# Optimization experiments

Measured on AMD Instinct MI355X. Metric: run time of the kernel, lower is better.

## Reference

```python
import jax, jax.numpy as jnp
import numpy as np

B, L, D, H = 2, 2048, 1024, 16
DH = D // H  # 64
SIGMA = float(np.sqrt(DH))  # sigma=None, learnable_sigma=False -> sqrt(d_head)


def setup_inputs() -> dict:
    key = jax.random.key(0)
    ks = jax.random.split(key, 5)
    x = jax.random.normal(ks[0], (B, L, D), dtype=jnp.float32)
    # causal visibility mask (1 = visible, 0 = masked), [B,1,L,L]
    mask = jnp.broadcast_to(jnp.tril(jnp.ones((L, L), jnp.int32))[None, None], (B, 1, L, L))
    scale = 0.02
    W_q = jax.random.normal(ks[1], (D, D), dtype=jnp.float32) * scale
    W_k = jax.random.normal(ks[2], (D, D), dtype=jnp.float32) * scale
    W_v = jax.random.normal(ks[3], (D, D), dtype=jnp.float32) * scale
    W_o = jax.random.normal(ks[4], (D, D), dtype=jnp.float32) * scale
    return {"x": x, "mask": mask, "W_q": W_q, "W_k": W_k, "W_v": W_v, "W_o": W_o}


def _split_heads(t):
    # [B,L,D] -> [B,H,L,DH]
    b, l, _ = t.shape
    return t.reshape(b, l, H, DH).transpose(0, 2, 1, 3)


def reference(x, mask, W_q, W_k, W_v, W_o):
    # nn.Linear(bias=False): y = x @ W.T
    Qh = _split_heads(x @ W_q.T)  # [B,H,L,DH]
    Kh = _split_heads(x @ W_k.T)
    Vh = _split_heads(x @ W_v.T)
    # RBF scores: -||q-k||^2 / (2 sigma^2)
    q_norm2 = jnp.sum(Qh * Qh, axis=-1, keepdims=True)          # [B,H,L,1]
    k_norm2 = jnp.sum(Kh * Kh, axis=-1)[..., None, :]            # [B,H,1,L]
    dot_qk = jnp.einsum('bhqd,bhkd->bhqk', Qh, Kh)               # [B,H,L,L]
    dist2 = q_norm2 + k_norm2 - 2.0 * dot_qk
    scores = -dist2 / (2.0 * SIGMA * SIGMA)
    scores = jnp.where(mask == 0, -jnp.inf, scores)
    attn = jax.nn.softmax(scores, axis=-1)
    Oh = jnp.einsum('bhqk,bhkd->bhqd', attn, Vh)                 # [B,H,L,DH]
    O = Oh.transpose(0, 2, 1, 3).reshape(B, L, D)
    return O @ W_o.T
```

## Files before the change

### kernel.cpp

```cpp
#include <hip/hip_runtime.h>

#define L_SEQ  2048
#define D_MODEL 1024
#define NH 16
#define DHEAD 64
#define BATCH 2

typedef __attribute__((ext_vector_type(8))) short bf16x8;
typedef __attribute__((ext_vector_type(4))) float f32x4;

__device__ inline ushort f2bf(float f) {
  unsigned int u = __builtin_bit_cast(unsigned int, f);
  return (ushort)((u + 0x7FFFu + ((u >> 16) & 1u)) >> 16);
}
__device__ inline float bf2f(ushort u) {
  return __builtin_bit_cast(float, (unsigned int)u << 16);
}

__device__ __forceinline__ void gload_lds16(const void* g, void* l) {
  __builtin_amdgcn_global_load_lds(
      (const __attribute__((address_space(1))) void*)g,
      (__attribute__((address_space(3))) void*)l, 16, 0, 0);
}

#define PROJ8 524288
#define WSZ8  131072
__global__ __launch_bounds__(256) void cvt_all(const float* __restrict__ x,
                                               const float* __restrict__ w0,
                                               const float* __restrict__ w1,
                                               const float* __restrict__ w2,
                                               const float* __restrict__ w3,
                                               ushort* __restrict__ xb,
                                               ushort* __restrict__ ob0,
                                               ushort* __restrict__ ob1,
                                               ushort* __restrict__ ob2,
                                               ushort* __restrict__ ob3) {
  const int gid = blockIdx.x * 256 + threadIdx.x;
  const float* in; ushort* out; int off;
  if (gid < PROJ8) { in = x; out = xb; off = gid; }
  else {
    const int j = gid - PROJ8;
    const int seg = j / WSZ8;
    off = j - seg * WSZ8;
    switch (seg) {
      case 0: in = w0; out = ob0; break;
      case 1: in = w1; out = ob1; break;
      case 2: in = w2; out = ob2; break;
      default: in = w3; out = ob3; break;
    }
  }
  const float4* p = (const float4*)in + (size_t)off * 2;
  const float4 a = p[0], b = p[1];
  ushort4 lo, hi;
  lo.x = f2bf(a.x); lo.y = f2bf(a.y); lo.z = f2bf(a.z); lo.w = f2bf(a.w);
  hi.x = f2bf(b.x); hi.y = f2bf(b.y); hi.z = f2bf(b.z); hi.w = f2bf(b.w);
  ((ushort4*)out)[(size_t)off * 2] = lo;
  ((ushort4*)out)[(size_t)off * 2 + 1] = hi;
}

__global__ __launch_bounds__(512, 2) void gemm8p(const ushort* __restrict__ A,
    const ushort* __restrict__ W0, const ushort* __restrict__ W1,
    const ushort* __restrict__ W2, ushort* __restrict__ Qb,
    ushort* __restrict__ Kb, ushort* __restrict__ Vtb) {
  __shared__ ushort As[2][2][128][64];
  __shared__ ushort Bs[2][2][128][64];
  const int tid = threadIdx.x;
  const int wid = tid >> 6, l = tid & 63, lr = l & 15, lg = l >> 4;
  const int wr = wid >> 2, wc = wid & 3;

  const int bid = blockIdx.x;
  const int swz = (bid & 7) * 24 + (bid >> 3);
  const int mt = swz / 12, nt_ = swz % 12;
  const int m0g = mt * 256;
  const ushort* W = (nt_ < 4) ? W0 : (nt_ < 8) ? W1 : W2;
  ushort* outQK = (nt_ < 4) ? Qb : Kb;
  const int mode2 = (nt_ >= 8);
  const int ncol0 = (nt_ & 3) * 256;

  const int srow = tid >> 3;
  const int schunk = (tid & 7) ^ (srow & 7);
  const ushort* Ag = A + (size_t)(m0g + srow) * D_MODEL + schunk * 8;
  const ushort* Wg = W + (size_t)(ncol0 + srow) * D_MODEL + schunk * 8;
  ushort* AsL = &As[0][0][0][0] + tid * 8;
  ushort* BsL = &Bs[0][0][0][0] + tid * 8;

#define STG_A(sl, h, T2)                                                        \
  {                                                                             \
    gload_lds16(Ag + (size_t)((h) * 128) * D_MODEL + (T2) * 64,                 \
                AsL + (sl) * 16384 + (h) * 8192);                               \
    gload_lds16(Ag + (size_t)((h) * 128 + 64) * D_MODEL + (T2) * 64,            \
                AsL + (sl) * 16384 + (h) * 8192 + 4096);                        \
  }
#define STG_B(sl, h, T2)                                                        \
  {                                                                             \
    gload_lds16(Wg + (size_t)((h) * 128) * D_MODEL + (T2) * 64,                 \
                BsL + (sl) * 16384 + (h) * 8192);                               \
    gload_lds16(Wg + (size_t)((h) * 128 + 64) * D_MODEL + (T2) * 64,            \
                BsL + (sl) * 16384 + (h) * 8192 + 4096);                        \
  }

  STG_A(0, 0, 0); STG_A(0, 1, 0); STG_B(0, 0, 0); STG_B(0, 1, 0);

  f32x4 acc[8][4] = {};
  bf16x8 bfr[4][2];
  const int NT = D_MODEL / 64;

#define PHASE(q)                                                                \
  {                                                                             \
    bf16x8 af[2][2];                                                            \
    _Pragma("unroll") for (int m2 = 0; m2 < 2; ++m2)                            \
      _Pragma("unroll") for (int kk = 0; kk < 2; ++kk)                          \
        af[m2][kk] = *(const bf16x8*)&As[s][wr][((q) * 2 + m2) * 16 + lr]       \
                                           [((kk * 4 + lg) ^ (lr & 7)) * 8];    \
    if (T + 1 < NT) {                                                           \
      if ((q) == 1)      { STG_A(s ^ 1, 1, T + 1); }                            \
      else if ((q) == 2) { STG_B(s ^ 1, 0, T + 1); }                            \
      else               { STG_B(s ^ 1, 1, T + 1); }                            \
    }                                                                           \
    __builtin_amdgcn_s_barrier();                                               \
    __builtin_amdgcn_s_setprio(1);                                              \
    _Pragma("unroll") for (int m2 = 0; m2 < 2; ++m2)                            \
      _Pragma("unroll") for (int kk = 0; kk < 2; ++kk)                          \
        _Pragma("unroll") for (int n = 0; n < 4; ++n)                           \
          acc[(q) * 2 + m2][n] = __builtin_amdgcn_mfma_f32_16x16x32_bf16(       \
              af[m2][kk], bfr[n][kk], acc[(q) * 2 + m2][n], 0, 0, 0);           \
    __builtin_amdgcn_s_setprio(0);                                              \
    __builtin_amdgcn_s_barrier();                                               \
  }

  for (int T = 0; T < NT; ++T) {
    const int s = T & 1;
    {
      if (T + 1 < NT) {
        STG_A(s ^ 1, 0, T + 1);
        asm volatile("s_waitcnt vmcnt(2)" ::: "memory");
      } else {
        asm volatile("s_waitcnt vmcnt(0)" ::: "memory");
      }
      __builtin_amdgcn_s_barrier();
#pragma unroll
      for (int n = 0; n < 4; ++n)
#pragma unroll
        for (int kk = 0; kk < 2; ++kk)
          bfr[n][kk] = *(const bf16x8*)&Bs[s][wc >> 1][(wc & 1) * 64 + n * 16 + lr]
                                          [((kk * 4 + lg) ^ (lr & 7)) * 8];
      bf16x8 af[2][2];
#pragma unroll
      for (int m2 = 0; m2 < 2; ++m2)
#pragma unroll
        for (int kk = 0; kk < 2; ++kk)
          af[m2][kk] = *(const bf16x8*)&As[s][wr][m2 * 16 + lr]
                                          [((kk * 4 + lg) ^ (lr & 7)) * 8];
      __builtin_amdgcn_s_setprio(1);
#pragma unroll
      for (int m2 = 0; m2 < 2; ++m2)
#pragma unroll
        for (int kk = 0; kk < 2; ++kk)
#pragma unroll
          for (int n = 0; n < 4; ++n)
            acc[m2][n] = __builtin_amdgcn_mfma_f32_16x16x32_bf16(
                af[m2][kk], bfr[n][kk], acc[m2][n], 0, 0, 0);
      __builtin_amdgcn_s_setprio(0);
      __builtin_amdgcn_s_barrier();
    }
    PHASE(1)
    PHASE(2)
    PHASE(3)
  }
#undef PHASE
#undef STG_A
#undef STG_B

  const int h = (nt_ & 3) * 4 + wc;
  if (!mode2) {
#pragma unroll
    for (int m = 0; m < 8; ++m)
#pragma unroll
      for (int r = 0; r < 4; ++r) {
        const int grow = m0g + wr * 128 + m * 16 + lg * 4 + r;
        const int b = grow >> 11, ll = grow & (L_SEQ - 1);
        ushort* dst = outQK + ((size_t)(b * NH + h) * L_SEQ + ll) * DHEAD;
#pragma unroll
        for (int n = 0; n < 4; ++n) dst[n * 16 + lr] = f2bf(acc[m][n][r]);
      }
  } else {
#pragma unroll
    for (int m = 0; m < 8; ++m) {
      const int grow0 = m0g + wr * 128 + m * 16 + lg * 4;
      const int b = grow0 >> 11, ll = grow0 & (L_SEQ - 1);
#pragma unroll
      for (int n = 0; n < 4; ++n) {
        ushort4 v;
        v.x = f2bf(acc[m][n][0]); v.y = f2bf(acc[m][n][1]);
        v.z = f2bf(acc[m][n][2]); v.w = f2bf(acc[m][n][3]);
        *(ushort4*)(Vtb + ((size_t)(b * NH + h) * DHEAD + n * 16 + lr) * L_SEQ + ll) = v;
      }
    }
  }
}

__global__ __launch_bounds__(256) void gemm128(const ushort* __restrict__ A,
    const ushort* __restrict__ W0, float* __restrict__ of) {
  __shared__ ushort As[2][128][32];
  __shared__ ushort Bs[2][128][32];
  const int tid = threadIdx.x;
  const int w = tid >> 6, l = tid & 63, lr = l & 15, lg = l >> 4;
  const int wr = w >> 1, wc = w & 1;

  const int cpx = gridDim.x >> 3;
  const int swz = (blockIdx.x & 7) * cpx + (blockIdx.x >> 3);
  const int ntile = swz % 8;
  const int m0 = (swz / 8) * 128;
  const int n0 = ntile * 128;

  const int srow = tid >> 2;
  const int skc_sw = (tid & 3) ^ (srow & 3);
  const ushort* Ag = A + (size_t)(m0 + srow) * D_MODEL + skc_sw * 8;
  const ushort* Wg = W0 + (size_t)(n0 + srow) * D_MODEL + skc_sw * 8;

#define STAGE(buf, k0)                                                      \
  {                                                                         \
    gload_lds16(Ag + (k0), &As[buf][0][0] + tid * 8);                       \
    gload_lds16(Ag + (size_t)64 * D_MODEL + (k0), &As[buf][0][0] + 2048 + tid * 8); \
    gload_lds16(Wg + (k0), &Bs[buf][0][0] + tid * 8);                       \
    gload_lds16(Wg + (size_t)64 * D_MODEL + (k0), &Bs[buf][0][0] + 2048 + tid * 8); \
  }

  STAGE(0, 0);

  f32x4 acc[4][4] = {};
  const int NT = D_MODEL / 32;
  for (int t = 0; t < NT; ++t) {
    const int cur = t & 1;
    if (t + 1 < NT) {
      STAGE(cur ^ 1, (t + 1) * 32);
      asm volatile("s_waitcnt vmcnt(4)" ::: "memory");
    } else {
      asm volatile("s_waitcnt vmcnt(0)" ::: "memory");
    }
    __builtin_amdgcn_s_barrier();

    bf16x8 af[4], bfv[4];
#pragma unroll
    for (int i = 0; i < 4; ++i)
      af[i] = *(const bf16x8*)&As[cur][wr * 64 + i * 16 + lr][(lg ^ (lr & 3)) * 8];
#pragma unroll
    for (int j = 0; j < 4; ++j)
      bfv[j] = *(const bf16x8*)&Bs[cur][wc * 64 + j * 16 + lr][(lg ^ (lr & 3)) * 8];
#pragma unroll
    for (int i = 0; i < 4; ++i)
#pragma unroll
      for (int j = 0; j < 4; ++j)
        acc[i][j] = __builtin_amdgcn_mfma_f32_16x16x32_bf16(af[i], bfv[j], acc[i][j], 0, 0, 0);
    __syncthreads();
  }
#undef STAGE

#pragma unroll
  for (int i = 0; i < 4; ++i)
#pragma unroll
    for (int r = 0; r < 4; ++r) {
      const int m = m0 + wr * 64 + i * 16 + lg * 4 + r;
#pragma unroll
      for (int j = 0; j < 4; ++j)
        of[(size_t)m * D_MODEL + n0 + wc * 64 + j * 16 + lr] = acc[i][j][r];
    }
}

__global__ __launch_bounds__(256) void kn_bf16(const ushort* __restrict__ K,
                                               float* __restrict__ Kn) {
  const int i = blockIdx.x * 256 + threadIdx.x;
  const ushort4* p = (const ushort4*)(K + (size_t)i * DHEAD);
  float s = 0.f;
#pragma unroll
  for (int j = 0; j < 16; ++j) {
    const ushort4 v = p[j];
    const float a = bf2f(v.x), b = bf2f(v.y), c = bf2f(v.z), d = bf2f(v.w);
    s += a * a + b * b + c * c + d * d;
  }
  Kn[i] = s * 0.011271055f;
}

__global__ __launch_bounds__(256, 3) void attn_mfma7(const ushort* __restrict__ Q,
                                                     const ushort* __restrict__ K,
                                                     const ushort* __restrict__ Vt,
                                                     const float* __restrict__ Kexp,
                                                     ushort* __restrict__ Ob) {
  const int blk = blockIdx.x;
  const int qb = 31 - (blk >> 5);
  const int bh = blk & 31;
  const int tid = threadIdx.x;
  const int w = tid >> 6, l = tid & 63, lr = l & 15, lg = l >> 4;
  const int q0w = qb * 64 + w * 16;
  const int nt = qb + 1;

  __shared__ ushort Ks[2][64][64];
  __shared__ ushort Vs[2][64][64];
  __shared__ ushort P[4][16][70];

  const size_t ho = (size_t)bh * L_SEQ * DHEAD;
  const ushort* Qh = Q + ho;
  const ushort* Kh = K + ho;
  const ushort* Vh = Vt + ho;
  const float* KeB = Kexp + (size_t)bh * L_SEQ;

  const bf16x8 qf0 = *(const bf16x8*)(Qh + (size_t)(q0w + lr) * DHEAD + lg * 8);
  const bf16x8 qf1 = *(const bf16x8*)(Qh + (size_t)(q0w + lr) * DHEAD + 32 + lg * 8);

  const int srow = tid >> 3;
  const int scs = (tid & 7) ^ (srow & 7);
  const ushort* Kg = Kh + (size_t)srow * DHEAD + scs * 8;
  const ushort* Vg = Vh + (size_t)srow * L_SEQ + scs * 8;
  const ushort* Kg2 = Kg + (size_t)32 * DHEAD;
  const ushort* Vg2 = Vg + (size_t)32 * L_SEQ;

#define STAGE_KV(buf, kb)                                                 \
  {                                                                       \
    gload_lds16(Kg + (size_t)(kb) * DHEAD, &Ks[buf][0][0] + tid * 8);     \
    gload_lds16(Kg2 + (size_t)(kb) * DHEAD, &Ks[buf][32][0] + tid * 8);   \
    gload_lds16(Vg + (kb), &Vs[buf][0][0] + tid * 8);                     \
    gload_lds16(Vg2 + (kb), &Vs[buf][32][0] + tid * 8);                   \
  }

#define TILE_QK(MASKED)                                                       \
    _Pragma("unroll")                                                         \
    for (int nf = 0; nf < 4; ++nf) {                                          \
      const int row = nf * 16 + lr;                                           \
      const bf16x8 kf0 = *(const bf16x8*)&Ks[cur][row][((lg) ^ (lr & 7)) * 8];\
      const bf16x8 kf1 = *(const bf16x8*)&Ks[cur][row][((4 + lg) ^ (lr & 7)) * 8];\
      f32x4 sv = {0.f, 0.f, 0.f, 0.f};                                        \
      sv = __builtin_amdgcn_mfma_f32_16x16x32_bf16(qf0, kf0, sv, 0, 0, 0);    \
      sv = __builtin_amdgcn_mfma_f32_16x16x32_bf16(qf1, kf1, sv, 0, 0, 0);    \
      const float keh = keC[nf];                                              \
      _Pragma("unroll")                                                       \
      for (int r = 0; r < 4; ++r) {                                           \
        float pv = __builtin_amdgcn_exp2f(fmaf(sv[r], 0.022542110f, -keh));   \
        if (MASKED && (kbase + row) > (q0w + lg * 4 + r)) pv = 0.f;           \
        P[w][lg * 4 + r][nf * 16 + lr] = f2bf(pv);                            \
      }                                                                       \
    }

  float keC[4], keN[4] = {0.f, 0.f, 0.f, 0.f};
#pragma unroll
  for (int nf = 0; nf < 4; ++nf) keC[nf] = KeB[nf * 16 + lr];
  STAGE_KV(0, 0);

  f32x4 oacc[4] = {};
  f32x4 lsacc = {};
  bf16x8 ones;
#pragma unroll
  for (int i = 0; i < 8; ++i) ones[i] = (short)0x3F80;

  for (int t = 0; t < nt; ++t) {
    const int cur = t & 1;
    if (t + 1 < nt) {
#pragma unroll
      for (int nf = 0; nf < 4; ++nf) keN[nf] = KeB[(t + 1) * 64 + nf * 16 + lr];
      asm volatile("" ::: "memory");
      STAGE_KV(cur ^ 1, (size_t)(t + 1) * 64);
      asm volatile("s_waitcnt vmcnt(4)" ::: "memory");
    } else {
      asm volatile("s_waitcnt vmcnt(0)" ::: "memory");
    }
    __builtin_amdgcn_s_barrier();

    const int kbase = t * 64;

    __builtin_amdgcn_s_setprio(1);
    if (t == qb) { TILE_QK(true) } else { TILE_QK(false) }
    const bf16x8 p0 = *(const bf16x8*)&P[w][lr][lg * 8];
    const bf16x8 p1 = *(const bf16x8*)&P[w][lr][32 + lg * 8];
    lsacc = __builtin_amdgcn_mfma_f32_16x16x32_bf16(p0, ones, lsacc, 0, 0, 0);
    lsacc = __builtin_amdgcn_mfma_f32_16x16x32_bf16(p1, ones, lsacc, 0, 0, 0);
#pragma unroll
    for (int nf = 0; nf < 4; ++nf) {
      const int row = nf * 16 + lr;
      const bf16x8 vf0 = *(const bf16x8*)&Vs[cur][row][((lg) ^ (lr & 7)) * 8];
      const bf16x8 vf1 = *(const bf16x8*)&Vs[cur][row][((4 + lg) ^ (lr & 7)) * 8];
      oacc[nf] = __builtin_amdgcn_mfma_f32_16x16x32_bf16(p0, vf0, oacc[nf], 0, 0, 0);
      oacc[nf] = __builtin_amdgcn_mfma_f32_16x16x32_bf16(p1, vf1, oacc[nf], 0, 0, 0);
    }
    __builtin_amdgcn_s_setprio(0);
    __builtin_amdgcn_s_barrier();
#pragma unroll
    for (int nf = 0; nf < 4; ++nf) keC[nf] = keN[nf];
  }
#undef STAGE_KV
#undef TILE_QK

  const int b = bh >> 4, h = bh & 15;
#pragma unroll
  for (int r = 0; r < 4; ++r) {
    const float inv = 1.0f / lsacc[r];
    const int q = q0w + lg * 4 + r;
#pragma unroll
    for (int nf = 0; nf < 4; ++nf)
      Ob[((size_t)(b * L_SEQ + q)) * D_MODEL + h * DHEAD + nf * 16 + lr] =
          f2bf(oacc[nf][r] * inv);
  }
}

extern "C" void kernel_launch(void* const* d_in, const int* in_sizes, int n_in,
                              void* d_out, int out_size, void* d_ws, size_t ws_size,
                              hipStream_t stream) {
  const float* x  = (const float*)d_in[0];
  const float* Wq = (const float*)d_in[2];
  const float* Wk = (const float*)d_in[3];
  const float* Wv = (const float*)d_in[4];
  const float* Wo = (const float*)d_in[5];

  const size_t PROJ = (size_t)BATCH * L_SEQ * D_MODEL;
  const size_t WSZ  = (size_t)D_MODEL * D_MODEL;
  ushort* xb  = (ushort*)d_ws;
  ushort* Wqb = xb + PROJ;
  ushort* Wkb = Wqb + WSZ;
  ushort* Wvb = Wkb + WSZ;
  ushort* Wob = Wvb + WSZ;
  ushort* Qb  = Wob + WSZ;
  ushort* Kb  = Qb + PROJ;
  ushort* Vtb = Kb + PROJ;
  ushort* Obf = Vtb + PROJ;
  float*  Kn  = (float*)(Obf + PROJ);

  cvt_all<<<(PROJ8 + 4 * WSZ8) / 256, 256, 0, stream>>>(x, Wq, Wk, Wv, Wo,
                                                        xb, Wqb, Wkb, Wvb, Wob);
  gemm8p<<<192, 512, 0, stream>>>(xb, Wqb, Wkb, Wvb, Qb, Kb, Vtb);
  kn_bf16<<<BATCH * NH * L_SEQ / 256, 256, 0, stream>>>(Kb, Kn);
  attn_mfma7<<<BATCH * NH * (L_SEQ / 64), 256, 0, stream>>>(Qb, Kb, Vtb, Kn, Obf);
  gemm128<<<256, 256, 0, stream>>>(Obf, Wob, (float*)d_out);
}
```

Baseline: 125.8 us.

## Double per-block query tile to 128 rows, two 16-row subtiles per wave

The attention kernel now processes 128 query rows per block, with each wave handling two 16-row query subtiles. Every staged K/V tile in LDS is therefore reused across twice as many queries, halving global K/V traffic and block count. Each wave skips tiles beyond its own causal boundary but still joins the barriers. The cost is more registers per wave (doubled accumulators and Q fragments), fewer blocks (512), and worse causal load imbalance within a block.

```diff
diff --git a/kernel.cpp b/kernel.cpp
--- a/kernel.cpp
+++ b/kernel.cpp
@@ -281,22 +281,23 @@
   Kn[i] = s * 0.011271055f;
 }
 
-__global__ __launch_bounds__(256, 3) void attn_mfma7(const ushort* __restrict__ Q,
+__global__ __launch_bounds__(256, 3) void attn_mfma8(const ushort* __restrict__ Q,
                                                      const ushort* __restrict__ K,
                                                      const ushort* __restrict__ Vt,
                                                      const float* __restrict__ Kexp,
                                                      ushort* __restrict__ Ob) {
   const int blk = blockIdx.x;
-  const int qb = 31 - (blk >> 5);
+  const int qb = 15 - (blk >> 5);
   const int bh = blk & 31;
   const int tid = threadIdx.x;
   const int w = tid >> 6, l = tid & 63, lr = l & 15, lg = l >> 4;
-  const int q0w = qb * 64 + w * 16;
-  const int nt = qb + 1;
+  const int q0w = qb * 128 + w * 32;
+  const int tbw = q0w >> 6;
+  const int ntmax = 2 * qb + 2;
 
   __shared__ ushort Ks[2][64][64];
   __shared__ ushort Vs[2][64][64];
-  __shared__ ushort P[4][16][70];
+  __shared__ ushort P[4][32][70];
 
   const size_t ho = (size_t)bh * L_SEQ * DHEAD;
   const ushort* Qh = Q + ho;
@@ -304,8 +305,13 @@
   const ushort* Vh = Vt + ho;
   const float* KeB = Kexp + (size_t)bh * L_SEQ;
 
-  const bf16x8 qf0 = *(const bf16x8*)(Qh + (size_t)(q0w + lr) * DHEAD + lg * 8);
-  const bf16x8 qf1 = *(const bf16x8*)(Qh + (size_t)(q0w + lr) * DHEAD + 32 + lg * 8);
+  bf16x8 qf[2][2];
+#pragma unroll
+  for (int qi = 0; qi < 2; ++qi)
+#pragma unroll
+    for (int kh = 0; kh < 2; ++kh)
+      qf[qi][kh] = *(const bf16x8*)(Qh + (size_t)(q0w + qi * 16 + lr) * DHEAD +
+                                    kh * 32 + lg * 8);
 
   const int srow = tid >> 3;
   const int scs = (tid & 7) ^ (srow & 7);
@@ -328,15 +334,18 @@
       const int row = nf * 16 + lr;                                           \
       const bf16x8 kf0 = *(const bf16x8*)&Ks[cur][row][((lg) ^ (lr & 7)) * 8];\
       const bf16x8 kf1 = *(const bf16x8*)&Ks[cur][row][((4 + lg) ^ (lr & 7)) * 8];\
-      f32x4 sv = {0.f, 0.f, 0.f, 0.f};                                        \
-      sv = __builtin_amdgcn_mfma_f32_16x16x32_bf16(qf0, kf0, sv, 0, 0, 0);    \
-      sv = __builtin_amdgcn_mfma_f32_16x16x32_bf16(qf1, kf1, sv, 0, 0, 0);    \
       const float keh = keC[nf];                                              \
       _Pragma("unroll")                                                       \
-      for (int r = 0; r < 4; ++r) {                                           \
-        float pv = __builtin_amdgcn_exp2f(fmaf(sv[r], 0.022542110f, -keh));   \
-        if (MASKED && (kbase + row) > (q0w + lg * 4 + r)) pv = 0.f;           \
-        P[w][lg * 4 + r][nf * 16 + lr] = f2bf(pv);                            \
+      for (int qi = 0; qi < 2; ++qi) {                                        \
+        f32x4 sv = {0.f, 0.f, 0.f, 0.f};                                      \
+        sv = __builtin_amdgcn_mfma_f32_16x16x32_bf16(qf[qi][0], kf0, sv, 0, 0, 0);\
+        sv = __builtin_amdgcn_mfma_f32_16x16x32_bf16(qf[qi][1], kf1, sv, 0, 0, 0);\
+        _Pragma("unroll")                                                     \
+        for (int r = 0; r < 4; ++r) {                                         \
+          float pv = __builtin_amdgcn_exp2f(fmaf(sv[r], 0.022542110f, -keh)); \
+          if (MASKED && (kbase + row) > (q0w + qi * 16 + lg * 4 + r)) pv = 0.f;\
+          P[w][qi * 16 + lg * 4 + r][nf * 16 + lr] = f2bf(pv);                \
+        }                                                                     \
       }                                                                       \
     }
 
@@ -345,15 +354,15 @@
   for (int nf = 0; nf < 4; ++nf) keC[nf] = KeB[nf * 16 + lr];
   STAGE_KV(0, 0);
 
-  f32x4 oacc[4] = {};
-  f32x4 lsacc = {};
+  f32x4 oacc[2][4] = {};
+  f32x4 lsacc[2] = {};
   bf16x8 ones;
 #pragma unroll
   for (int i = 0; i < 8; ++i) ones[i] = (short)0x3F80;
 
-  for (int t = 0; t < nt; ++t) {
+  for (int t = 0; t < ntmax; ++t) {
     const int cur = t & 1;
-    if (t + 1 < nt) {
+    if (t + 1 < ntmax) {
 #pragma unroll
       for (int nf = 0; nf < 4; ++nf) keN[nf] = KeB[(t + 1) * 64 + nf * 16 + lr];
       asm volatile("" ::: "memory");
@@ -366,21 +375,30 @@
 
     const int kbase = t * 64;
 
-    __builtin_amdgcn_s_setprio(1);
-    if (t == qb) { TILE_QK(true) } else { TILE_QK(false) }
-    const bf16x8 p0 = *(const bf16x8*)&P[w][lr][lg * 8];
-    const bf16x8 p1 = *(const bf16x8*)&P[w][lr][32 + lg * 8];
-    lsacc = __builtin_amdgcn_mfma_f32_16x16x32_bf16(p0, ones, lsacc, 0, 0, 0);
-    lsacc = __builtin_amdgcn_mfma_f32_16x16x32_bf16(p1, ones, lsacc, 0, 0, 0);
-#pragma unroll
-    for (int nf = 0; nf < 4; ++nf) {
-      const int row = nf * 16 + lr;
-      const bf16x8 vf0 = *(const bf16x8*)&Vs[cur][row][((lg) ^ (lr & 7)) * 8];
-      const bf16x8 vf1 = *(const bf16x8*)&Vs[cur][row][((4 + lg) ^ (lr & 7)) * 8];
-      oacc[nf] = __builtin_amdgcn_mfma_f32_16x16x32_bf16(p0, vf0, oacc[nf], 0, 0, 0);
-      oacc[nf] = __builtin_amdgcn_mfma_f32_16x16x32_bf16(p1, vf1, oacc[nf], 0, 0, 0);
-    }
-    __builtin_amdgcn_s_setprio(0);
+    if (t <= tbw) {
+      __builtin_amdgcn_s_setprio(1);
+      if (t == tbw) { TILE_QK(true) } else { TILE_QK(false) }
+      bf16x8 p0[2], p1[2];
+#pragma unroll
+      for (int qi = 0; qi < 2; ++qi) {
+        p0[qi] = *(const bf16x8*)&P[w][qi * 16 + lr][lg * 8];
+        p1[qi] = *(const bf16x8*)&P[w][qi * 16 + lr][32 + lg * 8];
+        lsacc[qi] = __builtin_amdgcn_mfma_f32_16x16x32_bf16(p0[qi], ones, lsacc[qi], 0, 0, 0);
+        lsacc[qi] = __builtin_amdgcn_mfma_f32_16x16x32_bf16(p1[qi], ones, lsacc[qi], 0, 0, 0);
+      }
+#pragma unroll
+      for (int nf = 0; nf < 4; ++nf) {
+        const int row = nf * 16 + lr;
+        const bf16x8 vf0 = *(const bf16x8*)&Vs[cur][row][((lg) ^ (lr & 7)) * 8];
+        const bf16x8 vf1 = *(const bf16x8*)&Vs[cur][row][((4 + lg) ^ (lr & 7)) * 8];
+#pragma unroll
+        for (int qi = 0; qi < 2; ++qi) {
+          oacc[qi][nf] = __builtin_amdgcn_mfma_f32_16x16x32_bf16(p0[qi], vf0, oacc[qi][nf], 0, 0, 0);
+          oacc[qi][nf] = __builtin_amdgcn_mfma_f32_16x16x32_bf16(p1[qi], vf1, oacc[qi][nf], 0, 0, 0);
+        }
+      }
+      __builtin_amdgcn_s_setprio(0);
+    }
     __builtin_amdgcn_s_barrier();
 #pragma unroll
     for (int nf = 0; nf < 4; ++nf) keC[nf] = keN[nf];
@@ -390,14 +408,16 @@
 
   const int b = bh >> 4, h = bh & 15;
 #pragma unroll
-  for (int r = 0; r < 4; ++r) {
-    const float inv = 1.0f / lsacc[r];
-    const int q = q0w + lg * 4 + r;
-#pragma unroll
-    for (int nf = 0; nf < 4; ++nf)
-      Ob[((size_t)(b * L_SEQ + q)) * D_MODEL + h * DHEAD + nf * 16 + lr] =
-          f2bf(oacc[nf][r] * inv);
-  }
+  for (int qi = 0; qi < 2; ++qi)
+#pragma unroll
+    for (int r = 0; r < 4; ++r) {
+      const float inv = 1.0f / lsacc[qi][r];
+      const int q = q0w + qi * 16 + lg * 4 + r;
+#pragma unroll
+      for (int nf = 0; nf < 4; ++nf)
+        Ob[((size_t)(b * L_SEQ + q)) * D_MODEL + h * DHEAD + nf * 16 + lr] =
+            f2bf(oacc[qi][nf][r] * inv);
+    }
 }
 
 extern "C" void kernel_launch(void* const* d_in, const int* in_sizes, int n_in,
@@ -426,6 +446,6 @@
                                                         xb, Wqb, Wkb, Wvb, Wob);
   gemm8p<<<192, 512, 0, stream>>>(xb, Wqb, Wkb, Wvb, Qb, Kb, Vtb);
   kn_bf16<<<BATCH * NH * L_SEQ / 256, 256, 0, stream>>>(Kb, Kn);
-  attn_mfma7<<<BATCH * NH * (L_SEQ / 64), 256, 0, stream>>>(Qb, Kb, Vtb, Kn, Obf);
+  attn_mfma8<<<BATCH * NH * (L_SEQ / 128), 256, 0, stream>>>(Qb, Kb, Vtb, Kn, Obf);
   gemm128<<<256, 256, 0, stream>>>(Obf, Wob, (float*)d_out);
 }
```

Measured after the change: 132.5 us. +5.4%, slower.

## Halve attention KV tile to 32 keys and skip per-wave fully masked tiles

Applied to the files above, without the earlier changes.

The attention kernel now streams K/V in 32-key tiles instead of 64, and each wave skips compute on tiles wholly above its own 16-row causal diagonal. This cuts wasted MFMA and exp work on masked regions and shrinks LDS so occupancy can rise to 4 blocks per CU. The cost is twice as many loop iterations and barriers per block, and waves idle while others finish diagonal tiles. The GEMM's trailing __syncthreads is also swapped for a raw s_barrier.

```diff
diff --git a/kernel.cpp b/kernel.cpp
--- a/kernel.cpp
+++ b/kernel.cpp
@@ -252,7 +252,7 @@
 #pragma unroll
       for (int j = 0; j < 4; ++j)
         acc[i][j] = __builtin_amdgcn_mfma_f32_16x16x32_bf16(af[i], bfv[j], acc[i][j], 0, 0, 0);
-    __syncthreads();
+    __builtin_amdgcn_s_barrier();
   }
 #undef STAGE
 
@@ -281,7 +281,7 @@
   Kn[i] = s * 0.011271055f;
 }
 
-__global__ __launch_bounds__(256, 3) void attn_mfma7(const ushort* __restrict__ Q,
+__global__ __launch_bounds__(256, 4) void attn_mfma9(const ushort* __restrict__ Q,
                                                      const ushort* __restrict__ K,
                                                      const ushort* __restrict__ Vt,
                                                      const float* __restrict__ Kexp,
@@ -292,11 +292,12 @@
   const int tid = threadIdx.x;
   const int w = tid >> 6, l = tid & 63, lr = l & 15, lg = l >> 4;
   const int q0w = qb * 64 + w * 16;
-  const int nt = qb + 1;
-
-  __shared__ ushort Ks[2][64][64];
-  __shared__ ushort Vs[2][64][64];
-  __shared__ ushort P[4][16][70];
+  const int tbw = q0w >> 5;
+  const int ntmax = 2 * qb + 2;
+
+  __shared__ ushort Ks[2][32][64];
+  __shared__ ushort Vs[2][64][32];
+  __shared__ ushort P[4][16][36];
 
   const size_t ho = (size_t)bh * L_SEQ * DHEAD;
   const ushort* Qh = Q + ho;
@@ -307,24 +308,22 @@
   const bf16x8 qf0 = *(const bf16x8*)(Qh + (size_t)(q0w + lr) * DHEAD + lg * 8);
   const bf16x8 qf1 = *(const bf16x8*)(Qh + (size_t)(q0w + lr) * DHEAD + 32 + lg * 8);
 
-  const int srow = tid >> 3;
-  const int scs = (tid & 7) ^ (srow & 7);
-  const ushort* Kg = Kh + (size_t)srow * DHEAD + scs * 8;
-  const ushort* Vg = Vh + (size_t)srow * L_SEQ + scs * 8;
-  const ushort* Kg2 = Kg + (size_t)32 * DHEAD;
-  const ushort* Vg2 = Vg + (size_t)32 * L_SEQ;
+  const int krow = tid >> 3;
+  const int kcs = (tid & 7) ^ (krow & 7);
+  const ushort* Kg = Kh + (size_t)krow * DHEAD + kcs * 8;
+  const int vrow = tid >> 2;
+  const int vcs = (tid & 3) ^ ((vrow >> 1) & 3);
+  const ushort* Vg = Vh + (size_t)vrow * L_SEQ + vcs * 8;
 
 #define STAGE_KV(buf, kb)                                                 \
   {                                                                       \
     gload_lds16(Kg + (size_t)(kb) * DHEAD, &Ks[buf][0][0] + tid * 8);     \
-    gload_lds16(Kg2 + (size_t)(kb) * DHEAD, &Ks[buf][32][0] + tid * 8);   \
     gload_lds16(Vg + (kb), &Vs[buf][0][0] + tid * 8);                     \
-    gload_lds16(Vg2 + (kb), &Vs[buf][32][0] + tid * 8);                   \
   }
 
 #define TILE_QK(MASKED)                                                       \
     _Pragma("unroll")                                                         \
-    for (int nf = 0; nf < 4; ++nf) {                                          \
+    for (int nf = 0; nf < 2; ++nf) {                                          \
       const int row = nf * 16 + lr;                                           \
       const bf16x8 kf0 = *(const bf16x8*)&Ks[cur][row][((lg) ^ (lr & 7)) * 8];\
       const bf16x8 kf1 = *(const bf16x8*)&Ks[cur][row][((4 + lg) ^ (lr & 7)) * 8];\
@@ -340,9 +339,9 @@
       }                                                                       \
     }
 
-  float keC[4], keN[4] = {0.f, 0.f, 0.f, 0.f};
-#pragma unroll
-  for (int nf = 0; nf < 4; ++nf) keC[nf] = KeB[nf * 16 + lr];
+  float keC[2], keN[2] = {0.f, 0.f};
+#pragma unroll
+  for (int nf = 0; nf < 2; ++nf) keC[nf] = KeB[nf * 16 + lr];
   STAGE_KV(0, 0);
 
   f32x4 oacc[4] = {};
@@ -351,39 +350,37 @@
 #pragma unroll
   for (int i = 0; i < 8; ++i) ones[i] = (short)0x3F80;
 
-  for (int t = 0; t < nt; ++t) {
+  for (int t = 0; t < ntmax; ++t) {
     const int cur = t & 1;
-    if (t + 1 < nt) {
-#pragma unroll
-      for (int nf = 0; nf < 4; ++nf) keN[nf] = KeB[(t + 1) * 64 + nf * 16 + lr];
+    if (t + 1 < ntmax) {
+#pragma unroll
+      for (int nf = 0; nf < 2; ++nf) keN[nf] = KeB[(t + 1) * 32 + nf * 16 + lr];
       asm volatile("" ::: "memory");
-      STAGE_KV(cur ^ 1, (size_t)(t + 1) * 64);
-      asm volatile("s_waitcnt vmcnt(4)" ::: "memory");
+      STAGE_KV(cur ^ 1, (size_t)(t + 1) * 32);
+      asm volatile("s_waitcnt vmcnt(2)" ::: "memory");
     } else {
       asm volatile("s_waitcnt vmcnt(0)" ::: "memory");
     }
     __builtin_amdgcn_s_barrier();
 
-    const int kbase = t * 64;
-
-    __builtin_amdgcn_s_setprio(1);
-    if (t == qb) { TILE_QK(true) } else { TILE_QK(false) }
-    const bf16x8 p0 = *(const bf16x8*)&P[w][lr][lg * 8];
-    const bf16x8 p1 = *(const bf16x8*)&P[w][lr][32 + lg * 8];
-    lsacc = __builtin_amdgcn_mfma_f32_16x16x32_bf16(p0, ones, lsacc, 0, 0, 0);
-    lsacc = __builtin_amdgcn_mfma_f32_16x16x32_bf16(p1, ones, lsacc, 0, 0, 0);
-#pragma unroll
-    for (int nf = 0; nf < 4; ++nf) {
-      const int row = nf * 16 + lr;
-      const bf16x8 vf0 = *(const bf16x8*)&Vs[cur][row][((lg) ^ (lr & 7)) * 8];
-      const bf16x8 vf1 = *(const bf16x8*)&Vs[cur][row][((4 + lg) ^ (lr & 7)) * 8];
-      oacc[nf] = __builtin_amdgcn_mfma_f32_16x16x32_bf16(p0, vf0, oacc[nf], 0, 0, 0);
-      oacc[nf] = __builtin_amdgcn_mfma_f32_16x16x32_bf16(p1, vf1, oacc[nf], 0, 0, 0);
-    }
-    __builtin_amdgcn_s_setprio(0);
+    const int kbase = t * 32;
+
+    if (t <= tbw) {
+      __builtin_amdgcn_s_setprio(1);
+      if (t == tbw) { TILE_QK(true) } else { TILE_QK(false) }
+      const bf16x8 pa = *(const bf16x8*)&P[w][lr][lg * 8];
+      lsacc = __builtin_amdgcn_mfma_f32_16x16x32_bf16(pa, ones, lsacc, 0, 0, 0);
+#pragma unroll
+      for (int nf = 0; nf < 4; ++nf) {
+        const int row = nf * 16 + lr;
+        const bf16x8 vf = *(const bf16x8*)&Vs[cur][row][((lg) ^ ((lr >> 1) & 3)) * 8];
+        oacc[nf] = __builtin_amdgcn_mfma_f32_16x16x32_bf16(pa, vf, oacc[nf], 0, 0, 0);
+      }
+      __builtin_amdgcn_s_setprio(0);
+    }
     __builtin_amdgcn_s_barrier();
 #pragma unroll
-    for (int nf = 0; nf < 4; ++nf) keC[nf] = keN[nf];
+    for (int nf = 0; nf < 2; ++nf) keC[nf] = keN[nf];
   }
 #undef STAGE_KV
 #undef TILE_QK
@@ -426,6 +423,6 @@
                                                         xb, Wqb, Wkb, Wvb, Wob);
   gemm8p<<<192, 512, 0, stream>>>(xb, Wqb, Wkb, Wvb, Qb, Kb, Vtb);
   kn_bf16<<<BATCH * NH * L_SEQ / 256, 256, 0, stream>>>(Kb, Kn);
-  attn_mfma7<<<BATCH * NH * (L_SEQ / 64), 256, 0, stream>>>(Qb, Kb, Vtb, Kn, Obf);
+  attn_mfma9<<<BATCH * NH * (L_SEQ / 64), 256, 0, stream>>>(Qb, Kb, Vtb, Kn, Obf);
   gemm128<<<256, 256, 0, stream>>>(Obf, Wob, (float*)d_out);
 }
```

New measurement: 136.5 us. +8.6%, slower.
